# Kernel optimization log

Measured on AMD Instinct MI355X. Metric: run time of the kernel, lower is better.

The kernel has to match this reference:

```python
import jax, jax.numpy as jnp
import numpy as np
from jax import lax

B_, S_, IN_, HID_ = 64, 512, 1024, 1024


def setup_inputs() -> dict:
    key = jax.random.key(0)
    k1, k2, k3, k4 = jax.random.split(key, 4)
    stdv = 1.0 / np.sqrt(HID_)
    return {
        "x": jax.random.normal(k1, (B_, S_, IN_), dtype=jnp.float32),
        "U": jax.random.uniform(k2, (IN_, 4 * HID_), minval=-stdv, maxval=stdv, dtype=jnp.float32),
        "V": jax.random.uniform(k3, (HID_, 4 * HID_), minval=-stdv, maxval=stdv, dtype=jnp.float32),
        "B": jax.random.uniform(k4, (4 * HID_,), minval=-stdv, maxval=stdv, dtype=jnp.float32),
        "h0": jnp.zeros((B_, HID_), dtype=jnp.float32),
        "c0": jnp.zeros((B_, HID_), dtype=jnp.float32),
    }


def reference(x, U, V, B, h0, c0):
    hd = h0.shape[-1]

    def step(carry, x_t):
        h, c = carry
        # [batch, 4*hid] combined gate pre-activation
        g = x_t @ U + h @ V + B
        n = jnp.tanh(g[:, 0:hd])                      # candidate (N_T)
        i = jax.nn.sigmoid(g[:, hd:2 * hd])           # input gate (I_T)
        f = jax.nn.sigmoid(g[:, 2 * hd:3 * hd])       # forget gate (F_T)
        o = jax.nn.sigmoid(g[:, 3 * hd:4 * hd])       # output gate (O_T)
        c_new = c * f + n * i                          # R_T
        h_new = jnp.tanh(c_new) * o                    # U_T
        return (h_new, c_new), h_new

    (h_fin, c_fin), ys = lax.scan(step, (h0, c0), jnp.swapaxes(x, 0, 1))
    out = jnp.swapaxes(ys, 0, 1)  # [batch, seq, hid]
    return out, (h_fin, c_fin)
```

## Files before the change

kernel.cpp:

```cpp
#include <hip/hip_runtime.h>
#include <stdint.h>


#define OUT_HF  33554432
#define OUT_CF  33619968

typedef __attribute__((ext_vector_type(8))) short bf16x8;
typedef __attribute__((ext_vector_type(4))) float f32x4;
typedef __attribute__((ext_vector_type(4))) unsigned short u16x4;
typedef __attribute__((ext_vector_type(4))) unsigned int u32x4;

#define WS_G    0
#define WS_XB   268435456
#define WS_HB   268435456
#define WS_FL   268959744
#define WS_UT   335544320

__device__ __forceinline__ unsigned short f2bf(float f) {
  unsigned u = __float_as_uint(f);
  u += 0x7FFFu + ((u >> 16) & 1u);
  return (unsigned short)(u >> 16);
}
__device__ __forceinline__ float bf2f(unsigned short b) {
  return __uint_as_float(((unsigned)b) << 16);
}
__device__ __forceinline__ float sigf(float x)   { return 1.0f / (1.0f + __expf(-x)); }
__device__ __forceinline__ float tanhf_(float x) { return 2.0f / (1.0f + __expf(-2.0f * x)) - 1.0f; }

__global__ void convert_x(const float* __restrict__ x, unsigned short* __restrict__ xb) {
  const int i = (blockIdx.x * 256 + threadIdx.x) * 4;
  f32x4 v = *(const f32x4*)(x + i);
  u16x4 o;
  o[0] = f2bf(v[0]); o[1] = f2bf(v[1]); o[2] = f2bf(v[2]); o[3] = f2bf(v[3]);
  *(u16x4*)(xb + i) = o;
}

__global__ void transpose_u(const float* __restrict__ U, unsigned short* __restrict__ ut) {
  __shared__ unsigned short t[64 * 65];
  const int kt = blockIdx.x;
  const int nt = blockIdx.y;
  const int tid = threadIdx.x;
  const int nn = tid & 63, kq = tid >> 6;
  #pragma unroll
  for (int i = 0; i < 16; ++i) {
    const int kk = kq * 16 + i;
    t[kk * 65 + nn] = f2bf(U[(size_t)(kt * 64 + kk) * 4096 + nt * 64 + nn]);
  }
  __syncthreads();
  const int kk2 = tid & 63, nq = tid >> 6;
  #pragma unroll
  for (int i = 0; i < 16; ++i) {
    const int nn2 = nq * 16 + i;
    ut[(size_t)(nt * 64 + nn2) * 1024 + kt * 64 + kk2] = t[kk2 * 65 + nn2];
  }
}

__global__ void init_h(const float* __restrict__ h0, uint32_t* __restrict__ hb32,
                       uint32_t* __restrict__ flags) {
  const int i = blockIdx.x * 256 + threadIdx.x;
  const uint32_t w0 = ((uint32_t)f2bf(h0[i])) << 16;
  const uint32_t w1 = 0xFFFFFFFFu;
  const uint32_t* p0 = hb32 + i;
  const uint32_t* p1 = hb32 + 65536 + i;
  asm volatile("global_store_dword %0, %2, off sc0 sc1\n\t"
               "global_store_dword %1, %3, off sc0 sc1"
               :: "v"(p0), "v"(p1), "v"(w0), "v"(w1) : "memory");
  if (i < 4096) {
    const uint32_t* fp = flags + i;
    const uint32_t z = 0u;
    asm volatile("global_store_dword %0, %1, off sc0 sc1"
                 :: "v"(fp), "v"(z) : "memory");
  }
}

__global__ void __launch_bounds__(256) gemm_xu(const unsigned short* __restrict__ A,
                                               const unsigned short* __restrict__ Bt,
                                               unsigned short* __restrict__ Gb) {
  __shared__ __align__(16) short As[4096];
  __shared__ __align__(16) short Bs[4096];
  const int tid = threadIdx.x;
  const int l = tid & 63, w = tid >> 6;
  const int wm = w & 1, wn = w >> 1;
  const int lm = l & 15, lq = l >> 4;
  const int bid = blockIdx.x;
  const int bm = bid & 255, bn = bid >> 8;

  const int i0 = tid >> 2, kc0 = tid & 3;
  const int la0 = (kc0 * 128 + (i0 ^ (kc0 << 2))) * 8;
  const int la1 = la0 + 512;
  const unsigned short* Ap = A  + (size_t)(bm * 128 + i0) * 1024 + kc0 * 8;
  const unsigned short* Bp = Bt + (size_t)(bn * 128 + i0) * 1024 + kc0 * 8;

  f32x4 acc[4][4] = {};

  for (int kt = 0; kt < 32; ++kt) {
    const int k0 = kt * 32;
    bf16x8 av0 = *(const bf16x8*)(Ap + k0);
    bf16x8 av1 = *(const bf16x8*)(Ap + 64 * 1024 + k0);
    bf16x8 bv0 = *(const bf16x8*)(Bp + k0);
    bf16x8 bv1 = *(const bf16x8*)(Bp + 64 * 1024 + k0);
    __syncthreads();
    *(bf16x8*)(As + la0) = av0;
    *(bf16x8*)(As + la1) = av1;
    *(bf16x8*)(Bs + la0) = bv0;
    *(bf16x8*)(Bs + la1) = bv1;
    __syncthreads();

    bf16x8 af[4], bfv[4];
    #pragma unroll
    for (int mt = 0; mt < 4; ++mt) {
      const int i = wm * 64 + mt * 16 + lm;
      af[mt] = *(const bf16x8*)(As + (lq * 128 + (i ^ (lq << 2))) * 8);
    }
    #pragma unroll
    for (int nt = 0; nt < 4; ++nt) {
      const int i = wn * 64 + nt * 16 + lm;
      bfv[nt] = *(const bf16x8*)(Bs + (lq * 128 + (i ^ (lq << 2))) * 8);
    }
    #pragma unroll
    for (int mt = 0; mt < 4; ++mt)
      #pragma unroll
      for (int nt = 0; nt < 4; ++nt)
        acc[mt][nt] = __builtin_amdgcn_mfma_f32_16x16x32_bf16(af[mt], bfv[nt], acc[mt][nt], 0, 0, 0);
  }

  #pragma unroll
  for (int mt = 0; mt < 4; ++mt)
    #pragma unroll
    for (int nt = 0; nt < 4; ++nt) {
      const int col = bn * 128 + wn * 64 + nt * 16 + lm;
      const int r0  = bm * 128 + wm * 64 + mt * 16 + lq * 4;
      #pragma unroll
      for (int r = 0; r < 4; ++r)
        Gb[(size_t)(r0 + r) * 4096 + col] = f2bf(acc[mt][nt][r]);
    }
}

__global__ void __launch_bounds__(256, 1) lstm_rec(
    const unsigned short* __restrict__ Gb,
    const float* __restrict__ V,
    const float* __restrict__ Bias,
    const float* __restrict__ c0,
    uint32_t* __restrict__ hb32,
    uint32_t* __restrict__ flags,
    float* __restrict__ out) {
  __shared__ __align__(16) float gbuf[4096];
  const int tid = threadIdx.x;
  const int l = tid & 63, w = tid >> 6;
  const int lm = l & 15, lq = l >> 4;
  const int bid = blockIdx.x;
  const int mb = bid & 3;
  const int nh = bid >> 2;
  const int jh = nh << 4;

  bf16x8 vf[8][4];
  {
    const int col0 = jh + lm;
    #pragma unroll
    for (int ks = 0; ks < 8; ++ks) {
      const int kb = (w << 8) + (ks << 5) + (lq << 3);
      #pragma unroll
      for (int g = 0; g < 4; ++g) {
        const size_t base = (size_t)kb * 4096 + (g << 10) + col0;
        bf16x8 v;
        #pragma unroll
        for (int jj = 0; jj < 8; ++jj)
          v[jj] = (short)f2bf(V[base + (size_t)jj * 4096]);
        vf[ks][g] = v;
      }
    }
  }

  const int b  = tid >> 4;
  const int j  = tid & 15;
  const int gr = (mb << 4) + b;
  float bias_r[4];
  #pragma unroll
  for (int g = 0; g < 4; ++g) bias_r[g] = Bias[(g << 10) + jh + j];
  float c = c0[(gr << 10) + jh + j];

  const int abase32 = ((mb << 4) + lm) * 1024 + (w << 8) + (lq << 3);
  const uint32_t* fwatch = flags + (((mb << 6) + l) << 4);
  const uint32_t* fmine  = flags + (((mb << 6) + nh) << 4);

  float gp[4], gn[4];
  {
    const size_t grow = (size_t)(gr << 9) * 4096;
    #pragma unroll
    for (int g = 0; g < 4; ++g) gp[g] = bf2f(Gb[grow + (g << 10) + jh + j]);
  }

  int budget = 20000000;

  for (int t = 0; t < 512; ++t) {
    {
      const int t2 = t < 511 ? t + 1 : t;
      const size_t grow = ((size_t)(gr << 9) + t2) * 4096;
      #pragma unroll
      for (int g = 0; g < 4; ++g) gn[g] = bf2f(Gb[grow + (g << 10) + jh + j]);
    }

    const uint32_t texp = (uint32_t)t;

    {
      uint32_t fv;
      do {
        asm volatile("global_load_dword %0, %1, off sc0 sc1\n\t"
                     "s_waitcnt vmcnt(0)"
                     : "=v"(fv) : "v"(fwatch) : "memory");
        if (__all(fv >= texp)) break;
        __builtin_amdgcn_s_sleep(2);
      } while (--budget > 0);
    }

    const uint32_t* hp = hb32 + ((t & 1) << 16) + abase32;
    u32x4 q0, q1, q2, q3, q4, q5, q6, q7, q8, q9, q10, q11, q12, q13, q14, q15;
    do {
      asm volatile(
          "global_load_dwordx4 %0, %16, off sc0 sc1\n\t"
          "global_load_dwordx4 %1, %16, off offset:16 sc0 sc1\n\t"
          "global_load_dwordx4 %2, %16, off offset:128 sc0 sc1\n\t"
          "global_load_dwordx4 %3, %16, off offset:144 sc0 sc1\n\t"
          "global_load_dwordx4 %4, %16, off offset:256 sc0 sc1\n\t"
          "global_load_dwordx4 %5, %16, off offset:272 sc0 sc1\n\t"
          "global_load_dwordx4 %6, %16, off offset:384 sc0 sc1\n\t"
          "global_load_dwordx4 %7, %16, off offset:400 sc0 sc1\n\t"
          "global_load_dwordx4 %8, %16, off offset:512 sc0 sc1\n\t"
          "global_load_dwordx4 %9, %16, off offset:528 sc0 sc1\n\t"
          "global_load_dwordx4 %10, %16, off offset:640 sc0 sc1\n\t"
          "global_load_dwordx4 %11, %16, off offset:656 sc0 sc1\n\t"
          "global_load_dwordx4 %12, %16, off offset:768 sc0 sc1\n\t"
          "global_load_dwordx4 %13, %16, off offset:784 sc0 sc1\n\t"
          "global_load_dwordx4 %14, %16, off offset:896 sc0 sc1\n\t"
          "global_load_dwordx4 %15, %16, off offset:912 sc0 sc1\n\t"
          "s_waitcnt vmcnt(0)"
          : "=&v"(q0), "=&v"(q1), "=&v"(q2), "=&v"(q3),
            "=&v"(q4), "=&v"(q5), "=&v"(q6), "=&v"(q7),
            "=&v"(q8), "=&v"(q9), "=&v"(q10), "=&v"(q11),
            "=&v"(q12), "=&v"(q13), "=&v"(q14), "=&v"(q15)
          : "v"(hp)
          : "memory");
      #define TC4(Q) ((Q[0] ^ texp) | (Q[1] ^ texp) | (Q[2] ^ texp) | (Q[3] ^ texp))
      const uint32_t dd = TC4(q0) | TC4(q1) | TC4(q2) | TC4(q3) |
                          TC4(q4) | TC4(q5) | TC4(q6) | TC4(q7) |
                          TC4(q8) | TC4(q9) | TC4(q10) | TC4(q11) |
                          TC4(q12) | TC4(q13) | TC4(q14) | TC4(q15);
      #undef TC4
      const int stale = (dd & 0xFFFFu) != 0;
      if (!__any(stale)) break;
      __builtin_amdgcn_s_sleep(2);
    } while (--budget > 0);

    bf16x8 a[8];
    #define MK(A, QA, QB) { u32x4 pa;                                     \
      pa[0] = __builtin_amdgcn_perm(QA[1], QA[0], 0x07060302u);           \
      pa[1] = __builtin_amdgcn_perm(QA[3], QA[2], 0x07060302u);           \
      pa[2] = __builtin_amdgcn_perm(QB[1], QB[0], 0x07060302u);           \
      pa[3] = __builtin_amdgcn_perm(QB[3], QB[2], 0x07060302u);           \
      A = __builtin_bit_cast(bf16x8, pa); }
    MK(a[0], q0, q1)  MK(a[1], q2, q3)  MK(a[2], q4, q5)  MK(a[3], q6, q7)
    MK(a[4], q8, q9)  MK(a[5], q10, q11) MK(a[6], q12, q13) MK(a[7], q14, q15)
    #undef MK

    f32x4 acc[4] = {};
    #pragma unroll
    for (int ks = 0; ks < 8; ++ks)
      #pragma unroll
      for (int g = 0; g < 4; ++g)
        acc[g] = __builtin_amdgcn_mfma_f32_16x16x32_bf16(a[ks], vf[ks][g], acc[g], 0, 0, 0);

    #pragma unroll
    for (int g = 0; g < 4; ++g)
      #pragma unroll
      for (int r = 0; r < 4; ++r)
        gbuf[((w << 8) + ((lq << 2) + r) * 16 + lm) * 4 + g] = acc[g][r];

    __syncthreads();

    f32x4 hv = *(const f32x4*)(gbuf + (tid << 2));
    hv += *(const f32x4*)(gbuf + ((256 + tid) << 2));
    hv += *(const f32x4*)(gbuf + ((512 + tid) << 2));
    hv += *(const f32x4*)(gbuf + ((768 + tid) << 2));

    const float pn = hv[0] + gp[0] + bias_r[0];
    const float pi = hv[1] + gp[1] + bias_r[1];
    const float pf = hv[2] + gp[2] + bias_r[2];
    const float po = hv[3] + gp[3] + bias_r[3];
    const float nn = tanhf_(pn);
    const float ii = sigf(pi);
    const float ff = sigf(pf);
    const float oo = sigf(po);
    c = c * ff + nn * ii;
    const float h = tanhf_(c) * oo;

    {
      const uint32_t* sp = hb32 + (((t + 1) & 1) << 16) + (gr << 10) + jh + j;
      const uint32_t hw = (((uint32_t)f2bf(h)) << 16) | ((uint32_t)(t + 1) & 0xFFFFu);
      asm volatile("global_store_dword %0, %1, off sc0 sc1"
                   :: "v"(sp), "v"(hw) : "memory");
    }

    asm volatile("s_waitcnt vmcnt(0)" ::: "memory");
    __syncthreads();
    if (tid == 0) {
      const uint32_t fw = (uint32_t)(t + 1);
      asm volatile("global_store_dword %0, %1, off sc0 sc1"
                   :: "v"(fmine), "v"(fw) : "memory");
    }

    out[(size_t)gr * 524288 + ((size_t)t << 10) + jh + j] = h;
    if (t == 511) {
      out[OUT_HF + (gr << 10) + jh + j] = h;
      out[OUT_CF + (gr << 10) + jh + j] = c;
    }
    #pragma unroll
    for (int g = 0; g < 4; ++g) gp[g] = gn[g];
  }
}

extern "C" void kernel_launch(void* const* d_in, const int* in_sizes, int n_in,
                              void* d_out, int out_size, void* d_ws, size_t ws_size,
                              hipStream_t stream) {
  const float* x  = (const float*)d_in[0];
  const float* U  = (const float*)d_in[1];
  const float* V  = (const float*)d_in[2];
  const float* Bi = (const float*)d_in[3];
  const float* h0 = (const float*)d_in[4];
  const float* c0 = (const float*)d_in[5];
  float* out = (float*)d_out;
  char* ws = (char*)d_ws;

  unsigned short* Gb = (unsigned short*)(ws + WS_G);
  unsigned short* xb = (unsigned short*)(ws + WS_XB);
  unsigned short* ut = (unsigned short*)(ws + WS_UT);
  uint32_t* hb32     = (uint32_t*)(ws + WS_HB);
  uint32_t* flg      = (uint32_t*)(ws + WS_FL);

  convert_x  <<<32768, 256, 0, stream>>>(x, xb);
  transpose_u<<<dim3(16, 64), 256, 0, stream>>>(U, ut);
  gemm_xu    <<<8192, 256, 0, stream>>>(xb, ut, Gb);
  init_h     <<<256, 256, 0, stream>>>(h0, hb32, flg);
  lstm_rec   <<<256, 256, 0, stream>>>(Gb, V, Bi, c0, hb32, flg, out);
}
```

Measured before the change: 2.877 ms.

## Interleave two batch groups per block in LSTM recurrence with deferred per-wave flags

The recurrent kernel now runs 128 blocks, each handling two 16-row batch groups in alternation, instead of 256 blocks handling one group each. The block's V fragment in registers is reused for both groups, so one group's flag wait and h load can overlap the other group's publish latency. Flags become per-wave entries in a packed 4-word layout that is read with a single dwordx4 load, and each flag store is deferred into the next slot's polling loop rather than waiting on vmcnt. The __syncthreads calls become raw s_barrier plus lgkmcnt waits. In exchange, half as many CUs do the recurrence, and the deferred, unsynchronised flag publication risks ordering errors.

```diff
diff --git a/kernel.cpp b/kernel.cpp
--- a/kernel.cpp
+++ b/kernel.cpp
@@ -65,7 +65,7 @@
   asm volatile("global_store_dword %0, %2, off sc0 sc1\n\t"
                "global_store_dword %1, %3, off sc0 sc1"
                :: "v"(p0), "v"(p1), "v"(w0), "v"(w1) : "memory");
-  if (i < 4096) {
+  if (i < 1024) {
     const uint32_t* fp = flags + i;
     const uint32_t z = 0u;
     asm volatile("global_store_dword %0, %1, off sc0 sc1"
@@ -134,6 +134,157 @@
       for (int r = 0; r < 4; ++r)
         Gb[(size_t)(r0 + r) * 4096 + col] = f2bf(acc[mt][nt][r]);
     }
+}
+
+__device__ __forceinline__ void lstm_slot(
+    const int t, const int grp, const int nh, const int jh,
+    const int tid, const int l, const int w, const int lm, const int lq,
+    const int b, const int j,
+    const unsigned short* __restrict__ Gb,
+    const bf16x8 (&vf)[8][4],
+    const float (&bias_r)[4],
+    float& c, float (&gp)[4],
+    uint32_t* __restrict__ hb32,
+    uint32_t* __restrict__ flags,
+    float* __restrict__ out,
+    float* gbuf,
+    int& budget, bool& pend, const uint32_t*& pendPtr, uint32_t& pendVal) {
+  const int gr = (grp << 4) + b;
+  const uint32_t texp = (uint32_t)t;
+
+  float gn[4];
+  {
+    const int t2 = t < 511 ? t + 1 : t;
+    const size_t grow = ((size_t)(gr << 9) + t2) * 4096;
+    #pragma unroll
+    for (int gg = 0; gg < 4; ++gg) gn[gg] = bf2f(Gb[grow + (gg << 10) + jh + j]);
+  }
+
+  {
+    const uint32_t* fwatch = flags + (((grp << 6) + l) << 2);
+    u32x4 fq;
+    do {
+      asm volatile("global_load_dwordx4 %0, %1, off sc0 sc1\n\t"
+                   "s_waitcnt vmcnt(0)"
+                   : "=&v"(fq) : "v"(fwatch) : "memory");
+      if (pend) {
+        if (l == 0)
+          asm volatile("global_store_dword %0, %1, off sc0 sc1"
+                       :: "v"(pendPtr), "v"(pendVal) : "memory");
+        pend = false;
+      }
+      const int ok = (fq[0] >= texp) & (fq[1] >= texp) & (fq[2] >= texp) & (fq[3] >= texp);
+      if (__all(ok)) break;
+      __builtin_amdgcn_s_sleep(2);
+    } while (--budget > 0);
+  }
+
+  const uint32_t* hp = hb32 + ((t & 1) << 16) + (((grp << 4) + lm) << 10) + (w << 8) + (lq << 3);
+  u32x4 q0, q1, q2, q3, q4, q5, q6, q7, q8, q9, q10, q11, q12, q13, q14, q15;
+  do {
+    asm volatile(
+        "global_load_dwordx4 %0, %16, off sc0 sc1\n\t"
+        "global_load_dwordx4 %1, %16, off offset:16 sc0 sc1\n\t"
+        "global_load_dwordx4 %2, %16, off offset:128 sc0 sc1\n\t"
+        "global_load_dwordx4 %3, %16, off offset:144 sc0 sc1\n\t"
+        "global_load_dwordx4 %4, %16, off offset:256 sc0 sc1\n\t"
+        "global_load_dwordx4 %5, %16, off offset:272 sc0 sc1\n\t"
+        "global_load_dwordx4 %6, %16, off offset:384 sc0 sc1\n\t"
+        "global_load_dwordx4 %7, %16, off offset:400 sc0 sc1\n\t"
+        "global_load_dwordx4 %8, %16, off offset:512 sc0 sc1\n\t"
+        "global_load_dwordx4 %9, %16, off offset:528 sc0 sc1\n\t"
+        "global_load_dwordx4 %10, %16, off offset:640 sc0 sc1\n\t"
+        "global_load_dwordx4 %11, %16, off offset:656 sc0 sc1\n\t"
+        "global_load_dwordx4 %12, %16, off offset:768 sc0 sc1\n\t"
+        "global_load_dwordx4 %13, %16, off offset:784 sc0 sc1\n\t"
+        "global_load_dwordx4 %14, %16, off offset:896 sc0 sc1\n\t"
+        "global_load_dwordx4 %15, %16, off offset:912 sc0 sc1\n\t"
+        "s_waitcnt vmcnt(0)"
+        : "=&v"(q0), "=&v"(q1), "=&v"(q2), "=&v"(q3),
+          "=&v"(q4), "=&v"(q5), "=&v"(q6), "=&v"(q7),
+          "=&v"(q8), "=&v"(q9), "=&v"(q10), "=&v"(q11),
+          "=&v"(q12), "=&v"(q13), "=&v"(q14), "=&v"(q15)
+        : "v"(hp)
+        : "memory");
+    #define TC4(Q) ((Q[0] ^ texp) | (Q[1] ^ texp) | (Q[2] ^ texp) | (Q[3] ^ texp))
+    const uint32_t dd = TC4(q0) | TC4(q1) | TC4(q2) | TC4(q3) |
+                        TC4(q4) | TC4(q5) | TC4(q6) | TC4(q7) |
+                        TC4(q8) | TC4(q9) | TC4(q10) | TC4(q11) |
+                        TC4(q12) | TC4(q13) | TC4(q14) | TC4(q15);
+    #undef TC4
+    const int stale = (dd & 0xFFFFu) != 0;
+    if (!__any(stale)) break;
+    __builtin_amdgcn_s_sleep(2);
+  } while (--budget > 0);
+
+  bf16x8 a[8];
+  #define MK(A, QA, QB) { u32x4 pa;                                     \
+    pa[0] = __builtin_amdgcn_perm(QA[1], QA[0], 0x07060302u);           \
+    pa[1] = __builtin_amdgcn_perm(QA[3], QA[2], 0x07060302u);           \
+    pa[2] = __builtin_amdgcn_perm(QB[1], QB[0], 0x07060302u);           \
+    pa[3] = __builtin_amdgcn_perm(QB[3], QB[2], 0x07060302u);           \
+    A = __builtin_bit_cast(bf16x8, pa); }
+  MK(a[0], q0, q1)  MK(a[1], q2, q3)  MK(a[2], q4, q5)  MK(a[3], q6, q7)
+  MK(a[4], q8, q9)  MK(a[5], q10, q11) MK(a[6], q12, q13) MK(a[7], q14, q15)
+  #undef MK
+
+  f32x4 acc[4] = {};
+  #pragma unroll
+  for (int ks = 0; ks < 8; ++ks)
+    #pragma unroll
+    for (int gg = 0; gg < 4; ++gg)
+      acc[gg] = __builtin_amdgcn_mfma_f32_16x16x32_bf16(a[ks], vf[ks][gg], acc[gg], 0, 0, 0);
+
+  #pragma unroll
+  for (int gg = 0; gg < 4; ++gg)
+    #pragma unroll
+    for (int r = 0; r < 4; ++r)
+      gbuf[((w << 8) + ((lq << 2) + r) * 16 + lm) * 4 + gg] = acc[gg][r];
+
+  asm volatile("s_waitcnt lgkmcnt(0)" ::: "memory");
+  __builtin_amdgcn_sched_barrier(0);
+  __builtin_amdgcn_s_barrier();
+  __builtin_amdgcn_sched_barrier(0);
+
+  f32x4 hv = *(const f32x4*)(gbuf + (tid << 2));
+  hv += *(const f32x4*)(gbuf + ((256 + tid) << 2));
+  hv += *(const f32x4*)(gbuf + ((512 + tid) << 2));
+  hv += *(const f32x4*)(gbuf + ((768 + tid) << 2));
+
+  const float pn = hv[0] + gp[0] + bias_r[0];
+  const float pi = hv[1] + gp[1] + bias_r[1];
+  const float pf = hv[2] + gp[2] + bias_r[2];
+  const float po = hv[3] + gp[3] + bias_r[3];
+  const float nn = tanhf_(pn);
+  const float ii = sigf(pi);
+  const float ff = sigf(pf);
+  const float oo = sigf(po);
+  c = c * ff + nn * ii;
+  const float h = tanhf_(c) * oo;
+
+  out[(size_t)gr * 524288 + ((size_t)t << 10) + jh + j] = h;
+
+  {
+    const uint32_t* sp = hb32 + (((t + 1) & 1) << 16) + ((size_t)(gr << 10)) + jh + j;
+    const uint32_t hw = (((uint32_t)f2bf(h)) << 16) | ((uint32_t)(t + 1) & 0xFFFFu);
+    asm volatile("global_store_dword %0, %1, off sc0 sc1"
+                 :: "v"(sp), "v"(hw) : "memory");
+  }
+
+  if (t == 511) {
+    out[OUT_HF + (gr << 10) + jh + j] = h;
+    out[OUT_CF + (gr << 10) + jh + j] = c;
+  }
+  #pragma unroll
+  for (int gg = 0; gg < 4; ++gg) gp[gg] = gn[gg];
+
+  pendPtr = flags + (((grp << 6) + nh) << 2) + w;
+  pendVal = (uint32_t)(t + 1);
+  pend = true;
+
+  __builtin_amdgcn_sched_barrier(0);
+  __builtin_amdgcn_s_barrier();
+  __builtin_amdgcn_sched_barrier(0);
 }
 
 __global__ void __launch_bounds__(256, 1) lstm_rec(
@@ -149,8 +300,9 @@
   const int l = tid & 63, w = tid >> 6;
   const int lm = l & 15, lq = l >> 4;
   const int bid = blockIdx.x;
-  const int mb = bid & 3;
-  const int nh = bid >> 2;
+  const int pr = bid >> 6;
+  const int g0 = pr << 1, g1 = g0 + 1;
+  const int nh = bid & 63;
   const int jh = nh << 4;
 
   bf16x8 vf[8][4];
@@ -160,161 +312,50 @@
     for (int ks = 0; ks < 8; ++ks) {
       const int kb = (w << 8) + (ks << 5) + (lq << 3);
       #pragma unroll
-      for (int g = 0; g < 4; ++g) {
-        const size_t base = (size_t)kb * 4096 + (g << 10) + col0;
+      for (int gg = 0; gg < 4; ++gg) {
+        const size_t base = (size_t)kb * 4096 + (gg << 10) + col0;
         bf16x8 v;
         #pragma unroll
         for (int jj = 0; jj < 8; ++jj)
           v[jj] = (short)f2bf(V[base + (size_t)jj * 4096]);
-        vf[ks][g] = v;
+        vf[ks][gg] = v;
       }
     }
   }
 
   const int b  = tid >> 4;
   const int j  = tid & 15;
-  const int gr = (mb << 4) + b;
+  const int gr0 = (g0 << 4) + b;
+  const int gr1 = (g1 << 4) + b;
   float bias_r[4];
   #pragma unroll
-  for (int g = 0; g < 4; ++g) bias_r[g] = Bias[(g << 10) + jh + j];
-  float c = c0[(gr << 10) + jh + j];
-
-  const int abase32 = ((mb << 4) + lm) * 1024 + (w << 8) + (lq << 3);
-  const uint32_t* fwatch = flags + (((mb << 6) + l) << 4);
-  const uint32_t* fmine  = flags + (((mb << 6) + nh) << 4);
-
-  float gp[4], gn[4];
-  {
-    const size_t grow = (size_t)(gr << 9) * 4096;
-    #pragma unroll
-    for (int g = 0; g < 4; ++g) gp[g] = bf2f(Gb[grow + (g << 10) + jh + j]);
+  for (int gg = 0; gg < 4; ++gg) bias_r[gg] = Bias[(gg << 10) + jh + j];
+  float cA = c0[(gr0 << 10) + jh + j];
+  float cB = c0[(gr1 << 10) + jh + j];
+
+  float gpA[4], gpB[4];
+  {
+    const size_t growA = (size_t)(gr0 << 9) * 4096;
+    const size_t growB = (size_t)(gr1 << 9) * 4096;
+    #pragma unroll
+    for (int gg = 0; gg < 4; ++gg) {
+      gpA[gg] = bf2f(Gb[growA + (gg << 10) + jh + j]);
+      gpB[gg] = bf2f(Gb[growB + (gg << 10) + jh + j]);
+    }
   }
 
   int budget = 20000000;
+  bool pend = false;
+  const uint32_t* pendPtr = nullptr;
+  uint32_t pendVal = 0;
 
   for (int t = 0; t < 512; ++t) {
-    {
-      const int t2 = t < 511 ? t + 1 : t;
-      const size_t grow = ((size_t)(gr << 9) + t2) * 4096;
-      #pragma unroll
-      for (int g = 0; g < 4; ++g) gn[g] = bf2f(Gb[grow + (g << 10) + jh + j]);
-    }
-
-    const uint32_t texp = (uint32_t)t;
-
-    {
-      uint32_t fv;
-      do {
-        asm volatile("global_load_dword %0, %1, off sc0 sc1\n\t"
-                     "s_waitcnt vmcnt(0)"
-                     : "=v"(fv) : "v"(fwatch) : "memory");
-        if (__all(fv >= texp)) break;
-        __builtin_amdgcn_s_sleep(2);
-      } while (--budget > 0);
-    }
-
-    const uint32_t* hp = hb32 + ((t & 1) << 16) + abase32;
-    u32x4 q0, q1, q2, q3, q4, q5, q6, q7, q8, q9, q10, q11, q12, q13, q14, q15;
-    do {
-      asm volatile(
-          "global_load_dwordx4 %0, %16, off sc0 sc1\n\t"
-          "global_load_dwordx4 %1, %16, off offset:16 sc0 sc1\n\t"
-          "global_load_dwordx4 %2, %16, off offset:128 sc0 sc1\n\t"
-          "global_load_dwordx4 %3, %16, off offset:144 sc0 sc1\n\t"
-          "global_load_dwordx4 %4, %16, off offset:256 sc0 sc1\n\t"
-          "global_load_dwordx4 %5, %16, off offset:272 sc0 sc1\n\t"
-          "global_load_dwordx4 %6, %16, off offset:384 sc0 sc1\n\t"
-          "global_load_dwordx4 %7, %16, off offset:400 sc0 sc1\n\t"
-          "global_load_dwordx4 %8, %16, off offset:512 sc0 sc1\n\t"
-          "global_load_dwordx4 %9, %16, off offset:528 sc0 sc1\n\t"
-          "global_load_dwordx4 %10, %16, off offset:640 sc0 sc1\n\t"
-          "global_load_dwordx4 %11, %16, off offset:656 sc0 sc1\n\t"
-          "global_load_dwordx4 %12, %16, off offset:768 sc0 sc1\n\t"
-          "global_load_dwordx4 %13, %16, off offset:784 sc0 sc1\n\t"
-          "global_load_dwordx4 %14, %16, off offset:896 sc0 sc1\n\t"
-          "global_load_dwordx4 %15, %16, off offset:912 sc0 sc1\n\t"
-          "s_waitcnt vmcnt(0)"
-          : "=&v"(q0), "=&v"(q1), "=&v"(q2), "=&v"(q3),
-            "=&v"(q4), "=&v"(q5), "=&v"(q6), "=&v"(q7),
-            "=&v"(q8), "=&v"(q9), "=&v"(q10), "=&v"(q11),
-            "=&v"(q12), "=&v"(q13), "=&v"(q14), "=&v"(q15)
-          : "v"(hp)
-          : "memory");
-      #define TC4(Q) ((Q[0] ^ texp) | (Q[1] ^ texp) | (Q[2] ^ texp) | (Q[3] ^ texp))
-      const uint32_t dd = TC4(q0) | TC4(q1) | TC4(q2) | TC4(q3) |
-                          TC4(q4) | TC4(q5) | TC4(q6) | TC4(q7) |
-                          TC4(q8) | TC4(q9) | TC4(q10) | TC4(q11) |
-                          TC4(q12) | TC4(q13) | TC4(q14) | TC4(q15);
-      #undef TC4
-      const int stale = (dd & 0xFFFFu) != 0;
-      if (!__any(stale)) break;
-      __builtin_amdgcn_s_sleep(2);
-    } while (--budget > 0);
-
-    bf16x8 a[8];
-    #define MK(A, QA, QB) { u32x4 pa;                                     \
-      pa[0] = __builtin_amdgcn_perm(QA[1], QA[0], 0x07060302u);           \
-      pa[1] = __builtin_amdgcn_perm(QA[3], QA[2], 0x07060302u);           \
-      pa[2] = __builtin_amdgcn_perm(QB[1], QB[0], 0x07060302u);           \
-      pa[3] = __builtin_amdgcn_perm(QB[3], QB[2], 0x07060302u);           \
-      A = __builtin_bit_cast(bf16x8, pa); }
-    MK(a[0], q0, q1)  MK(a[1], q2, q3)  MK(a[2], q4, q5)  MK(a[3], q6, q7)
-    MK(a[4], q8, q9)  MK(a[5], q10, q11) MK(a[6], q12, q13) MK(a[7], q14, q15)
-    #undef MK
-
-    f32x4 acc[4] = {};
-    #pragma unroll
-    for (int ks = 0; ks < 8; ++ks)
-      #pragma unroll
-      for (int g = 0; g < 4; ++g)
-        acc[g] = __builtin_amdgcn_mfma_f32_16x16x32_bf16(a[ks], vf[ks][g], acc[g], 0, 0, 0);
-
-    #pragma unroll
-    for (int g = 0; g < 4; ++g)
-      #pragma unroll
-      for (int r = 0; r < 4; ++r)
-        gbuf[((w << 8) + ((lq << 2) + r) * 16 + lm) * 4 + g] = acc[g][r];
-
-    __syncthreads();
-
-    f32x4 hv = *(const f32x4*)(gbuf + (tid << 2));
-    hv += *(const f32x4*)(gbuf + ((256 + tid) << 2));
-    hv += *(const f32x4*)(gbuf + ((512 + tid) << 2));
-    hv += *(const f32x4*)(gbuf + ((768 + tid) << 2));
-
-    const float pn = hv[0] + gp[0] + bias_r[0];
-    const float pi = hv[1] + gp[1] + bias_r[1];
-    const float pf = hv[2] + gp[2] + bias_r[2];
-    const float po = hv[3] + gp[3] + bias_r[3];
-    const float nn = tanhf_(pn);
-    const float ii = sigf(pi);
-    const float ff = sigf(pf);
-    const float oo = sigf(po);
-    c = c * ff + nn * ii;
-    const float h = tanhf_(c) * oo;
-
-    {
-      const uint32_t* sp = hb32 + (((t + 1) & 1) << 16) + (gr << 10) + jh + j;
-      const uint32_t hw = (((uint32_t)f2bf(h)) << 16) | ((uint32_t)(t + 1) & 0xFFFFu);
-      asm volatile("global_store_dword %0, %1, off sc0 sc1"
-                   :: "v"(sp), "v"(hw) : "memory");
-    }
-
-    asm volatile("s_waitcnt vmcnt(0)" ::: "memory");
-    __syncthreads();
-    if (tid == 0) {
-      const uint32_t fw = (uint32_t)(t + 1);
-      asm volatile("global_store_dword %0, %1, off sc0 sc1"
-                   :: "v"(fmine), "v"(fw) : "memory");
-    }
-
-    out[(size_t)gr * 524288 + ((size_t)t << 10) + jh + j] = h;
-    if (t == 511) {
-      out[OUT_HF + (gr << 10) + jh + j] = h;
-      out[OUT_CF + (gr << 10) + jh + j] = c;
-    }
-    #pragma unroll
-    for (int g = 0; g < 4; ++g) gp[g] = gn[g];
+    lstm_slot(t, g0, nh, jh, tid, l, w, lm, lq, b, j,
+              Gb, vf, bias_r, cA, gpA, hb32, flags, out, gbuf,
+              budget, pend, pendPtr, pendVal);
+    lstm_slot(t, g1, nh, jh, tid, l, w, lm, lq, b, j,
+              Gb, vf, bias_r, cB, gpB, hb32, flags, out, gbuf,
+              budget, pend, pendPtr, pendVal);
   }
 }
 
@@ -340,5 +381,5 @@
   transpose_u<<<dim3(16, 64), 256, 0, stream>>>(U, ut);
   gemm_xu    <<<8192, 256, 0, stream>>>(xb, ut, Gb);
   init_h     <<<256, 256, 0, stream>>>(h0, hb32, flg);
-  lstm_rec   <<<256, 256, 0, stream>>>(Gb, V, Bi, c0, hb32, flg, out);
-}
+  lstm_rec   <<<128, 256, 0, stream>>>(Gb, V, Bi, c0, hb32, flg, out);
+}
```

Result: slower. 4.380 ms (+52.2%).

## Repartition recurrent LSTM blocks to 8 rows × 32 columns with 8 waves each

Applied to the files above, without the earlier changes.

Changes the persistent recurrent kernel from 4 batch groups × 64 column slices of 16 to 8 batch groups of 8 rows × 32 column slices of 32, using 512 threads (8 waves) per block, each wave covering 128 of K. Only 8 h rows are needed per block, so each lane loads a quarter of the previous h data. A ds_swizzle then splits the MFMA 16-row A operand between real rows and duplicates. Each block now syncs with 32 rather than 64 producer flags, at the cost of half-wasted MFMA rows, an 8-way LDS reduction, and only half the threads doing the cell update.

```diff
diff --git a/kernel.cpp b/kernel.cpp
--- a/kernel.cpp
+++ b/kernel.cpp
@@ -136,7 +136,7 @@
     }
 }
 
-__global__ void __launch_bounds__(256, 1) lstm_rec(
+__global__ void __launch_bounds__(512, 1) lstm_rec(
     const unsigned short* __restrict__ Gb,
     const float* __restrict__ V,
     const float* __restrict__ Bias,
@@ -144,63 +144,69 @@
     uint32_t* __restrict__ hb32,
     uint32_t* __restrict__ flags,
     float* __restrict__ out) {
-  __shared__ __align__(16) float gbuf[4096];
+  __shared__ __align__(16) float gbuf[8192];
   const int tid = threadIdx.x;
   const int l = tid & 63, w = tid >> 6;
-  const int lm = l & 15, lq = l >> 4;
+  const int lm = l & 15;
+  const int kq = l >> 4;
   const int bid = blockIdx.x;
-  const int mb = bid & 3;
-  const int nh = bid >> 2;
-  const int jh = nh << 4;
-
-  bf16x8 vf[8][4];
+  const int mb = bid & 7;
+  const int nh = bid >> 3;
+  const int jh = nh << 5;
+
+  bf16x8 vf[4][4][2];
   {
-    const int col0 = jh + lm;
-    #pragma unroll
-    for (int ks = 0; ks < 8; ++ks) {
-      const int kb = (w << 8) + (ks << 5) + (lq << 3);
-      #pragma unroll
-      for (int g = 0; g < 4; ++g) {
-        const size_t base = (size_t)kb * 4096 + (g << 10) + col0;
-        bf16x8 v;
+    #pragma unroll
+    for (int ks = 0; ks < 4; ++ks) {
+      const int kb = (w << 7) + (ks << 5) + (kq << 3);
+      #pragma unroll
+      for (int g = 0; g < 4; ++g)
         #pragma unroll
-        for (int jj = 0; jj < 8; ++jj)
-          v[jj] = (short)f2bf(V[base + (size_t)jj * 4096]);
-        vf[ks][g] = v;
-      }
-    }
-  }
-
-  const int b  = tid >> 4;
-  const int j  = tid & 15;
-  const int gr = (mb << 4) + b;
+        for (int ct = 0; ct < 2; ++ct) {
+          const size_t base = (size_t)kb * 4096 + (g << 10) + jh + (ct << 4) + lm;
+          bf16x8 v;
+          #pragma unroll
+          for (int jj = 0; jj < 8; ++jj)
+            v[jj] = (short)f2bf(V[base + (size_t)jj * 4096]);
+          vf[ks][g][ct] = v;
+        }
+    }
+  }
+
+  const int b  = (tid >> 5) & 7;
+  const int cc = tid & 31;
+  const int gr = (mb << 3) + b;
+  const bool cellown = tid < 256;
   float bias_r[4];
   #pragma unroll
-  for (int g = 0; g < 4; ++g) bias_r[g] = Bias[(g << 10) + jh + j];
-  float c = c0[(gr << 10) + jh + j];
-
-  const int abase32 = ((mb << 4) + lm) * 1024 + (w << 8) + (lq << 3);
-  const uint32_t* fwatch = flags + (((mb << 6) + l) << 4);
-  const uint32_t* fmine  = flags + (((mb << 6) + nh) << 4);
+  for (int g = 0; g < 4; ++g) bias_r[g] = Bias[(g << 10) + jh + cc];
+  float c = cellown ? c0[(gr << 10) + jh + cc] : 0.0f;
+
+  const int abase32 = ((mb << 3) + (l & 7)) * 1024 + (w << 7) + (((l >> 3) & 1) << 6) + (kq << 3);
+  const bool hi = (l & 8) != 0;
+
+  const uint32_t* fwatch = flags + (((mb << 5) + (l & 31)) << 4);
+  const uint32_t* fmine  = flags + (((mb << 5) + nh) << 4);
 
   float gp[4], gn[4];
-  {
+  if (cellown) {
     const size_t grow = (size_t)(gr << 9) * 4096;
     #pragma unroll
-    for (int g = 0; g < 4; ++g) gp[g] = bf2f(Gb[grow + (g << 10) + jh + j]);
+    for (int g = 0; g < 4; ++g) gp[g] = bf2f(Gb[grow + (g << 10) + jh + cc]);
   }
 
   int budget = 20000000;
 
   for (int t = 0; t < 512; ++t) {
-    {
+    if (cellown) {
       const int t2 = t < 511 ? t + 1 : t;
       const size_t grow = ((size_t)(gr << 9) + t2) * 4096;
       #pragma unroll
-      for (int g = 0; g < 4; ++g) gn[g] = bf2f(Gb[grow + (g << 10) + jh + j]);
+      for (int g = 0; g < 4; ++g) gn[g] = bf2f(Gb[grow + (g << 10) + jh + cc]);
     }
 
     const uint32_t texp = (uint32_t)t;
+    const uint32_t* bufb = hb32 + ((t & 1) << 16);
 
     {
       uint32_t fv;
@@ -213,91 +219,101 @@
       } while (--budget > 0);
     }
 
-    const uint32_t* hp = hb32 + ((t & 1) << 16) + abase32;
-    u32x4 q0, q1, q2, q3, q4, q5, q6, q7, q8, q9, q10, q11, q12, q13, q14, q15;
+    const uint32_t* hp = bufb + abase32;
+    u32x4 r0, r1, r2, r3;
     do {
       asm volatile(
-          "global_load_dwordx4 %0, %16, off sc0 sc1\n\t"
-          "global_load_dwordx4 %1, %16, off offset:16 sc0 sc1\n\t"
-          "global_load_dwordx4 %2, %16, off offset:128 sc0 sc1\n\t"
-          "global_load_dwordx4 %3, %16, off offset:144 sc0 sc1\n\t"
-          "global_load_dwordx4 %4, %16, off offset:256 sc0 sc1\n\t"
-          "global_load_dwordx4 %5, %16, off offset:272 sc0 sc1\n\t"
-          "global_load_dwordx4 %6, %16, off offset:384 sc0 sc1\n\t"
-          "global_load_dwordx4 %7, %16, off offset:400 sc0 sc1\n\t"
-          "global_load_dwordx4 %8, %16, off offset:512 sc0 sc1\n\t"
-          "global_load_dwordx4 %9, %16, off offset:528 sc0 sc1\n\t"
-          "global_load_dwordx4 %10, %16, off offset:640 sc0 sc1\n\t"
-          "global_load_dwordx4 %11, %16, off offset:656 sc0 sc1\n\t"
-          "global_load_dwordx4 %12, %16, off offset:768 sc0 sc1\n\t"
-          "global_load_dwordx4 %13, %16, off offset:784 sc0 sc1\n\t"
-          "global_load_dwordx4 %14, %16, off offset:896 sc0 sc1\n\t"
-          "global_load_dwordx4 %15, %16, off offset:912 sc0 sc1\n\t"
+          "global_load_dwordx4 %0, %4, off sc0 sc1\n\t"
+          "global_load_dwordx4 %1, %4, off offset:16 sc0 sc1\n\t"
+          "global_load_dwordx4 %2, %4, off offset:128 sc0 sc1\n\t"
+          "global_load_dwordx4 %3, %4, off offset:144 sc0 sc1\n\t"
           "s_waitcnt vmcnt(0)"
-          : "=&v"(q0), "=&v"(q1), "=&v"(q2), "=&v"(q3),
-            "=&v"(q4), "=&v"(q5), "=&v"(q6), "=&v"(q7),
-            "=&v"(q8), "=&v"(q9), "=&v"(q10), "=&v"(q11),
-            "=&v"(q12), "=&v"(q13), "=&v"(q14), "=&v"(q15)
+          : "=&v"(r0), "=&v"(r1), "=&v"(r2), "=&v"(r3)
           : "v"(hp)
           : "memory");
       #define TC4(Q) ((Q[0] ^ texp) | (Q[1] ^ texp) | (Q[2] ^ texp) | (Q[3] ^ texp))
-      const uint32_t dd = TC4(q0) | TC4(q1) | TC4(q2) | TC4(q3) |
-                          TC4(q4) | TC4(q5) | TC4(q6) | TC4(q7) |
-                          TC4(q8) | TC4(q9) | TC4(q10) | TC4(q11) |
-                          TC4(q12) | TC4(q13) | TC4(q14) | TC4(q15);
+      const uint32_t dd = TC4(r0) | TC4(r1) | TC4(r2) | TC4(r3);
       #undef TC4
       const int stale = (dd & 0xFFFFu) != 0;
       if (!__any(stale)) break;
       __builtin_amdgcn_s_sleep(2);
     } while (--budget > 0);
 
-    bf16x8 a[8];
+    u32x4 s0, s1, s2, s3;
+    #define SWZ(D, S) { \
+      D[0] = (unsigned)__builtin_amdgcn_ds_swizzle((int)S[0], 0x201F); \
+      D[1] = (unsigned)__builtin_amdgcn_ds_swizzle((int)S[1], 0x201F); \
+      D[2] = (unsigned)__builtin_amdgcn_ds_swizzle((int)S[2], 0x201F); \
+      D[3] = (unsigned)__builtin_amdgcn_ds_swizzle((int)S[3], 0x201F); }
+    SWZ(s0, r0) SWZ(s1, r1) SWZ(s2, r2) SWZ(s3, r3)
+    #undef SWZ
+    u32x4 qa0 = hi ? s0 : r0, qa1 = hi ? s1 : r1;
+    u32x4 qa2 = hi ? s2 : r2, qa3 = hi ? s3 : r3;
+    u32x4 qb0 = hi ? r0 : s0, qb1 = hi ? r1 : s1;
+    u32x4 qb2 = hi ? r2 : s2, qb3 = hi ? r3 : s3;
+
+    bf16x8 a0, a1, a2, a3;
     #define MK(A, QA, QB) { u32x4 pa;                                     \
       pa[0] = __builtin_amdgcn_perm(QA[1], QA[0], 0x07060302u);           \
       pa[1] = __builtin_amdgcn_perm(QA[3], QA[2], 0x07060302u);           \
       pa[2] = __builtin_amdgcn_perm(QB[1], QB[0], 0x07060302u);           \
       pa[3] = __builtin_amdgcn_perm(QB[3], QB[2], 0x07060302u);           \
       A = __builtin_bit_cast(bf16x8, pa); }
-    MK(a[0], q0, q1)  MK(a[1], q2, q3)  MK(a[2], q4, q5)  MK(a[3], q6, q7)
-    MK(a[4], q8, q9)  MK(a[5], q10, q11) MK(a[6], q12, q13) MK(a[7], q14, q15)
+    MK(a0, qa0, qa1)  MK(a1, qa2, qa3)  MK(a2, qb0, qb1)  MK(a3, qb2, qb3)
     #undef MK
 
-    f32x4 acc[4] = {};
-    #pragma unroll
-    for (int ks = 0; ks < 8; ++ks)
-      #pragma unroll
-      for (int g = 0; g < 4; ++g)
-        acc[g] = __builtin_amdgcn_mfma_f32_16x16x32_bf16(a[ks], vf[ks][g], acc[g], 0, 0, 0);
-
-    #pragma unroll
-    for (int g = 0; g < 4; ++g)
-      #pragma unroll
-      for (int r = 0; r < 4; ++r)
-        gbuf[((w << 8) + ((lq << 2) + r) * 16 + lm) * 4 + g] = acc[g][r];
+    f32x4 acc[2][4] = {};
+    #define DOKS(A, KS)                                                               \
+      _Pragma("unroll")                                                               \
+      for (int g = 0; g < 4; ++g) {                                                   \
+        acc[0][g] = __builtin_amdgcn_mfma_f32_16x16x32_bf16(A, vf[KS][g][0], acc[0][g], 0, 0, 0); \
+        acc[1][g] = __builtin_amdgcn_mfma_f32_16x16x32_bf16(A, vf[KS][g][1], acc[1][g], 0, 0, 0); \
+      }
+    DOKS(a0, 0) DOKS(a1, 1) DOKS(a2, 2) DOKS(a3, 3)
+    #undef DOKS
+
+    if (kq < 2) {
+      #pragma unroll
+      for (int ct = 0; ct < 2; ++ct)
+        #pragma unroll
+        for (int g = 0; g < 4; ++g)
+          #pragma unroll
+          for (int r = 0; r < 4; ++r)
+            gbuf[(w << 10) + (((kq << 2) + r) << 7) + (((ct << 4) + lm) << 2) + g] = acc[ct][g][r];
+    }
 
     __syncthreads();
 
-    f32x4 hv = *(const f32x4*)(gbuf + (tid << 2));
-    hv += *(const f32x4*)(gbuf + ((256 + tid) << 2));
-    hv += *(const f32x4*)(gbuf + ((512 + tid) << 2));
-    hv += *(const f32x4*)(gbuf + ((768 + tid) << 2));
-
-    const float pn = hv[0] + gp[0] + bias_r[0];
-    const float pi = hv[1] + gp[1] + bias_r[1];
-    const float pf = hv[2] + gp[2] + bias_r[2];
-    const float po = hv[3] + gp[3] + bias_r[3];
-    const float nn = tanhf_(pn);
-    const float ii = sigf(pi);
-    const float ff = sigf(pf);
-    const float oo = sigf(po);
-    c = c * ff + nn * ii;
-    const float h = tanhf_(c) * oo;
-
-    {
-      const uint32_t* sp = hb32 + (((t + 1) & 1) << 16) + (gr << 10) + jh + j;
+    if (cellown) {
+      const int off = (b << 7) + (cc << 2);
+      f32x4 hv = *(const f32x4*)(gbuf + off);
+      #pragma unroll
+      for (int w2 = 1; w2 < 8; ++w2)
+        hv += *(const f32x4*)(gbuf + (w2 << 10) + off);
+
+      const float pn = hv[0] + gp[0] + bias_r[0];
+      const float pi = hv[1] + gp[1] + bias_r[1];
+      const float pf = hv[2] + gp[2] + bias_r[2];
+      const float po = hv[3] + gp[3] + bias_r[3];
+      const float nn = tanhf_(pn);
+      const float ii = sigf(pi);
+      const float ff = sigf(pf);
+      const float oo = sigf(po);
+      c = c * ff + nn * ii;
+      const float h = tanhf_(c) * oo;
+
+      const uint32_t* sp = hb32 + (((t + 1) & 1) << 16) + (gr << 10) + jh + cc;
       const uint32_t hw = (((uint32_t)f2bf(h)) << 16) | ((uint32_t)(t + 1) & 0xFFFFu);
       asm volatile("global_store_dword %0, %1, off sc0 sc1"
                    :: "v"(sp), "v"(hw) : "memory");
+
+      out[(size_t)gr * 524288 + ((size_t)t << 10) + jh + cc] = h;
+      if (t == 511) {
+        out[OUT_HF + (gr << 10) + jh + cc] = h;
+        out[OUT_CF + (gr << 10) + jh + cc] = c;
+      }
+      #pragma unroll
+      for (int g = 0; g < 4; ++g) gp[g] = gn[g];
     }
 
     asm volatile("s_waitcnt vmcnt(0)" ::: "memory");
@@ -307,14 +323,6 @@
       asm volatile("global_store_dword %0, %1, off sc0 sc1"
                    :: "v"(fmine), "v"(fw) : "memory");
     }
-
-    out[(size_t)gr * 524288 + ((size_t)t << 10) + jh + j] = h;
-    if (t == 511) {
-      out[OUT_HF + (gr << 10) + jh + j] = h;
-      out[OUT_CF + (gr << 10) + jh + j] = c;
-    }
-    #pragma unroll
-    for (int g = 0; g < 4; ++g) gp[g] = gn[g];
   }
 }
 
@@ -340,5 +348,5 @@
   transpose_u<<<dim3(16, 64), 256, 0, stream>>>(U, ut);
   gemm_xu    <<<8192, 256, 0, stream>>>(xb, ut, Gb);
   init_h     <<<256, 256, 0, stream>>>(h0, hb32, flg);
-  lstm_rec   <<<256, 256, 0, stream>>>(Gb, V, Bi, c0, hb32, flg, out);
-}
+  lstm_rec   <<<256, 512, 0, stream>>>(Gb, V, Bi, c0, hb32, flg, out);
+}
```

After: 2.605 ms. 1.1x faster.
